# Optimization experiments

Measured on AMD Instinct MI355X. Metric: run time of the kernel, lower is better.

Reference implementation:

```python
import jax, jax.numpy as jnp
import numpy as np

EMB_DIM = 1024
SEQ = 2048
BATCH = 4


def setup_inputs() -> dict:
    key = jax.random.key(0)
    k1, k2, k3, k4, k5 = jax.random.split(key, 5)
    Q = jax.random.normal(k1, (SEQ, BATCH, EMB_DIM), dtype=jnp.float32)
    K = jax.random.normal(k2, (SEQ, BATCH, EMB_DIM), dtype=jnp.float32)
    V = jax.random.normal(k3, (SEQ, BATCH, EMB_DIM), dtype=jnp.float32)
    # nn.Linear default init scale ~ 1/sqrt(fan_in)
    W_in = jax.random.normal(k4, (3 * EMB_DIM, EMB_DIM), dtype=jnp.float32) / np.sqrt(EMB_DIM)
    W_out = jax.random.normal(k5, (EMB_DIM, EMB_DIM), dtype=jnp.float32) / np.sqrt(EMB_DIM)
    return {"Q": Q, "K": K, "V": V, "W_in": W_in, "W_out": W_out}


def reference(Q, K, V, W_in, W_out):
    # NOTE: original module ignores K and V args entirely (self-attention on Q).
    emb = Q.shape[-1]
    scale = 1.0 / np.sqrt(emb)
    qkv = jnp.einsum('sbe,fe->sbf', Q, W_in)        # [S, B, 3E]
    q, k, v = jnp.split(qkv, 3, axis=-1)            # each [S, B, E]
    q = jnp.transpose(q, (1, 0, 2)) * scale         # [B, S, E]
    k = jnp.transpose(k, (1, 0, 2))                 # [B, S, E]
    v = jnp.transpose(v, (1, 0, 2))                 # [B, S, E]
    scores = jnp.einsum('bte,bse->bts', q, k)       # [B, T, S]
    # per-target-row softmax over source dim == vectorized softmax on last axis
    weights = jax.nn.softmax(scores, axis=-1)       # [B, T, S]
    out = jnp.einsum('bts,bse->bte', weights, v)    # [B, T, E]
    out = jnp.transpose(out, (1, 0, 2))             # [T, B, E]
    out = jnp.einsum('tbe,fe->tbf', out, W_out)     # [T, B, E]
    return (out, weights)
```

## Files before the change

### kernel.cpp

```cpp
#include <hip/hip_runtime.h>
#include <stdint.h>

typedef unsigned short u16;
typedef __bf16 bf16_t;
typedef bf16_t bf16x8 __attribute__((ext_vector_type(8)));
typedef float f32x4 __attribute__((ext_vector_type(4)));
typedef u16 u16x4 __attribute__((ext_vector_type(4)));
typedef u16 u16x8 __attribute__((ext_vector_type(8)));

#define AS1 __attribute__((address_space(1)))
#define AS3 __attribute__((address_space(3)))

__device__ __forceinline__ u16 f2bf(float f) {
  union { float f; uint32_t u; } x; x.f = f;
  uint32_t u = x.u;
  return (u16)((u + 0x7fffu + ((u >> 16) & 1u)) >> 16);
}

__device__ __forceinline__ float bf2f(u16 b) {
  union { uint32_t u; float f; } x; x.u = ((uint32_t)b) << 16;
  return x.f;
}

__device__ __forceinline__ void gload_lds16(const void* g, void* lds) {
  __builtin_amdgcn_global_load_lds((const AS1 uint32_t*)g, (AS3 uint32_t*)lds, 16, 0, 0);
}

__device__ __forceinline__ void xcd_remap(int& bx, int& by, int& bz) {
  const int gx = gridDim.x, gy = gridDim.y;
  const int n = gx * gy * gridDim.z;
  const int lin = blockIdx.x + gx * (blockIdx.y + gy * blockIdx.z);
  const int q = n >> 3;
  const int work = (lin & 7) * q + (lin >> 3);
  bx = work % gx;
  const int t = work / gx;
  by = t % gy;
  bz = t / gy;
}

#define BARRIER() do { asm volatile("" ::: "memory"); \
                       __builtin_amdgcn_s_barrier();  \
                       asm volatile("" ::: "memory"); } while (0)

#define MQS(MQi, NQi, ASET, BSET)                                              \
  do {                                                                         \
    __builtin_amdgcn_s_setprio(1);                                             \
    _Pragma("unroll") for (int j_ = 0; j_ < 4; ++j_) {                         \
      _Pragma("unroll") for (int i_ = 0; i_ < 2; ++i_) {                       \
        acc[(MQi) * 4 + j_][(NQi) * 2 + i_] =                                  \
            __builtin_amdgcn_mfma_f32_16x16x32_bf16(                           \
                ASET[j_][0], BSET[i_][0],                                      \
                acc[(MQi) * 4 + j_][(NQi) * 2 + i_], 0, 0, 0);                 \
        acc[(MQi) * 4 + j_][(NQi) * 2 + i_] =                                  \
            __builtin_amdgcn_mfma_f32_16x16x32_bf16(                           \
                ASET[j_][1], BSET[i_][1],                                      \
                acc[(MQi) * 4 + j_][(NQi) * 2 + i_], 0, 0, 0);                 \
      }                                                                        \
    }                                                                          \
    __builtin_amdgcn_s_setprio(0);                                             \
  } while (0)

__global__ __launch_bounds__(256)
void cvt3(const float* __restrict__ Q, const float* __restrict__ Wi,
          const float* __restrict__ Wo, u16* __restrict__ Qb,
          u16* __restrict__ Wib, u16* __restrict__ Wob) {
  const int i = blockIdx.x * 256 + threadIdx.x;
  const float* src;
  u16* dst;
  int j;
  if (i < 2097152)            { src = Q;  dst = Qb;  j = i; }
  else if (i < 2883584)       { src = Wi; dst = Wib; j = i - 2097152; }
  else                        { src = Wo; dst = Wob; j = i - 2883584; }
  float4 v = ((const float4*)src)[j];
  u16x4 o = {f2bf(v.x), f2bf(v.y), f2bf(v.z), f2bf(v.w)};
  *(u16x4*)(dst + (size_t)j * 4) = o;
}

template <bool BF16OUT>
__global__ __launch_bounds__(512, 2)
void gemm256(const u16* __restrict__ A, const u16* __restrict__ B,
             void* __restrict__ Cv,
             int lda, int ldb, int ldc,
             long long sAz, long long sBz, long long sCz,
             int K, float alpha) {
  __shared__ u16 As[2][256 * 64];
  __shared__ u16 Bs[2][256 * 64];
  int bx, by, bz;
  xcd_remap(bx, by, bz);
  const int tid  = threadIdx.x;
  const int lane = tid & 63;
  const int wid  = tid >> 6;
  const int wr   = wid >> 2;
  const int wc   = wid & 3;
  const long long z = bz;
  const u16* Ab = A + z * sAz;
  const u16* Bb = B + z * sBz;
  const int rowBase = by * 256;
  const int colBase = bx * 256;
  const int nt = K >> 6;

  const int sRow   = tid >> 3;
  const int sChunk = (tid & 7) ^ (sRow & 7);
  const size_t ldaS = (size_t)lda, ldbS = (size_t)ldb;
  const u16* aS = Ab + (size_t)(rowBase + sRow) * ldaS + sChunk * 8;
  const u16* bS = Bb + (size_t)(colBase + sRow) * ldbS + sChunk * 8;

  const int fr = lane & 15;
  const int kx = lane >> 4;
  const int rx = lane & 7;

  f32x4 acc[8][4];
  const f32x4 zf = {0.f, 0.f, 0.f, 0.f};
#pragma unroll
  for (int m = 0; m < 8; ++m)
#pragma unroll
    for (int n = 0; n < 4; ++n) acc[m][n] = zf;

  bf16x8 Ara[4][2], Arb[4][2], Bra[2][2], Brb[2][2];

  auto stageA = [&](int buf, int h, int kt) {
    const u16* s = aS + (size_t)(h * 128) * ldaS + kt;
    char* d = ((char*)&As[buf][0]) + h * 16384 + tid * 16;
    gload_lds16(s, d);
    gload_lds16(s + 64 * ldaS, d + 8192);
  };
  auto stageB = [&](int buf, int h, int kt) {
    const u16* s = bS + (size_t)(h * 128) * ldbS + kt;
    char* d = ((char*)&Bs[buf][0]) + h * 16384 + tid * 16;
    gload_lds16(s, d);
    gload_lds16(s + 64 * ldbS, d + 8192);
  };
  auto ldsA = [&](int buf, int mq, bf16x8 (&dst)[4][2]) {
#pragma unroll
    for (int j = 0; j < 4; ++j) {
      const int row = mq * 128 + wr * 64 + j * 16 + fr;
#pragma unroll
      for (int k = 0; k < 2; ++k) {
        const int ch = ((k * 4 + kx) ^ rx) * 8;
        dst[j][k] = *(const bf16x8*)&As[buf][row * 64 + ch];
      }
    }
  };
  auto ldsB = [&](int buf, int nq, bf16x8 (&dst)[2][2]) {
#pragma unroll
    for (int i = 0; i < 2; ++i) {
      const int row = nq * 128 + i * 64 + wc * 16 + fr;
#pragma unroll
      for (int k = 0; k < 2; ++k) {
        const int ch = ((k * 4 + kx) ^ rx) * 8;
        dst[i][k] = *(const bf16x8*)&Bs[buf][row * 64 + ch];
      }
    }
  };

  stageA(0, 0, 0);
  stageA(0, 1, 0);
  stageB(0, 0, 0);
  stageB(0, 1, 0);
  asm volatile("s_waitcnt vmcnt(0)" ::: "memory");
  BARRIER();
  ldsA(0, 0, Ara);
  ldsB(0, 0, Bra);

  for (int t = 0; t < nt; ++t) {
    const int c = t & 1;
    const int kt1 = (t + 1) << 6;
    const bool s1 = (t + 1 < nt);
    ldsB(c, 1, Brb);
    ldsA(c, 1, Arb);
    if (s1) {
      stageA(1 - c, 0, kt1);
      stageA(1 - c, 1, kt1);
      stageB(1 - c, 0, kt1);
      stageB(1 - c, 1, kt1);
    }
    MQS(0, 0, Ara, Bra);
    MQS(0, 1, Ara, Brb);
    if (s1) {
      asm volatile("s_waitcnt lgkmcnt(0)" ::: "memory");
      asm volatile("s_waitcnt vmcnt(0)" ::: "memory");
      BARRIER();
      ldsA(1 - c, 0, Ara);
      __builtin_amdgcn_sched_barrier(0);
    }
    MQS(1, 0, Arb, Bra);
    if (s1) ldsB(1 - c, 0, Bra);
    MQS(1, 1, Arb, Brb);
  }

  const int r0 = (lane >> 4) * 4;
#pragma unroll
  for (int m = 0; m < 8; ++m) {
    const int grow = rowBase + (m >> 2) * 128 + wr * 64 + (m & 3) * 16 + r0;
#pragma unroll
    for (int jj = 0; jj < 4; ++jj) {
      const size_t rOff = (size_t)(grow + jj) * (size_t)ldc;
      if constexpr (BF16OUT) {
        u16* C = (u16*)Cv + z * sCz;
#pragma unroll
        for (int n = 0; n < 4; ++n) {
          const int gcol = colBase + (n >> 1) * 128 + (n & 1) * 64 + wc * 16 + fr;
          C[rOff + gcol] = f2bf(acc[m][n][jj] * alpha);
        }
      } else {
        float* C = (float*)Cv + z * sCz;
#pragma unroll
        for (int n = 0; n < 4; ++n) {
          const int gcol = colBase + (n >> 1) * 128 + (n & 1) * 64 + wc * 16 + fr;
          C[rOff + gcol] = acc[m][n][jj] * alpha;
        }
      }
    }
  }
}

template <bool BF16OUT>
__global__ __launch_bounds__(512, 2)
void gemm128(const u16* __restrict__ A, const u16* __restrict__ B,
             void* __restrict__ Cv,
             int lda, int ldb, int ldc,
             long long sAz, long long sBz, long long sCz,
             int K, float alpha) {
  __shared__ u16 As[2][128 * 64];
  __shared__ u16 Bs[2][256 * 64];
  int bx, by, bz;
  xcd_remap(bx, by, bz);
  const int tid  = threadIdx.x;
  const int lane = tid & 63;
  const int wid  = tid >> 6;
  const int wr   = wid >> 2;
  const int wc   = wid & 3;
  const long long z = bz;
  const u16* Ab = A + z * sAz;
  const u16* Bb = B + z * sBz;
  const int rowBase = by * 128;
  const int colBase = bx * 256;
  const int nt = K >> 6;

  const int sRow   = tid >> 3;
  const int sChunk = (tid & 7) ^ (sRow & 7);
  const size_t ldaS = (size_t)lda, ldbS = (size_t)ldb;
  const u16* aS = Ab + (size_t)(rowBase + sRow) * ldaS + sChunk * 8;
  const u16* bS = Bb + (size_t)(colBase + sRow) * ldbS + sChunk * 8;

  const int fr = lane & 15;
  const int kx = lane >> 4;
  const int rx = lane & 7;

  f32x4 acc[4][4];
  const f32x4 zf = {0.f, 0.f, 0.f, 0.f};
#pragma unroll
  for (int m = 0; m < 4; ++m)
#pragma unroll
    for (int n = 0; n < 4; ++n) acc[m][n] = zf;

  bf16x8 Ara[4][2], Arb[4][2], Bra[2][2], Brb[2][2];

  auto stageA = [&](int buf, int kt) {
    const u16* s = aS + kt;
    char* d = ((char*)&As[buf][0]) + tid * 16;
    gload_lds16(s, d);
    gload_lds16(s + 64 * ldaS, d + 8192);
  };
  auto stageB = [&](int buf, int h, int kt) {
    const u16* s = bS + (size_t)(h * 128) * ldbS + kt;
    char* d = ((char*)&Bs[buf][0]) + h * 16384 + tid * 16;
    gload_lds16(s, d);
    gload_lds16(s + 64 * ldbS, d + 8192);
  };
  auto ldsA = [&](int buf, bf16x8 (&dst)[4][2]) {
#pragma unroll
    for (int j = 0; j < 4; ++j) {
      const int row = wr * 64 + j * 16 + fr;
#pragma unroll
      for (int k = 0; k < 2; ++k) {
        const int ch = ((k * 4 + kx) ^ rx) * 8;
        dst[j][k] = *(const bf16x8*)&As[buf][row * 64 + ch];
      }
    }
  };
  auto ldsB = [&](int buf, int nq, bf16x8 (&dst)[2][2]) {
#pragma unroll
    for (int i = 0; i < 2; ++i) {
      const int row = nq * 128 + i * 64 + wc * 16 + fr;
#pragma unroll
      for (int k = 0; k < 2; ++k) {
        const int ch = ((k * 4 + kx) ^ rx) * 8;
        dst[i][k] = *(const bf16x8*)&Bs[buf][row * 64 + ch];
      }
    }
  };

  auto tile = [&](int t, int c, bf16x8 (&ACUR)[4][2], bf16x8 (&ANXT)[4][2]) {
    const int kt1 = (t + 1) << 6;
    const bool s1 = (t + 1 < nt);
    ldsB(c, 1, Brb);
    if (s1) {
      stageA(1 - c, kt1);
      stageB(1 - c, 0, kt1);
      stageB(1 - c, 1, kt1);
    }
    MQS(0, 0, ACUR, Bra);
    if (s1) {
      asm volatile("s_waitcnt lgkmcnt(0)" ::: "memory");
      asm volatile("s_waitcnt vmcnt(0)" ::: "memory");
      BARRIER();
      ldsA(1 - c, ANXT);
      ldsB(1 - c, 0, Bra);
      __builtin_amdgcn_sched_barrier(0);
    }
    MQS(0, 1, ACUR, Brb);
  };

  stageA(0, 0);
  stageB(0, 0, 0);
  stageB(0, 1, 0);
  asm volatile("s_waitcnt vmcnt(0)" ::: "memory");
  BARRIER();
  ldsA(0, Ara);
  ldsB(0, 0, Bra);

  for (int tt = 0; tt < nt; tt += 2) {
    tile(tt,     0, Ara, Arb);
    tile(tt + 1, 1, Arb, Ara);
  }

  const int r0 = (lane >> 4) * 4;
#pragma unroll
  for (int m = 0; m < 4; ++m) {
    const int grow = rowBase + wr * 64 + m * 16 + r0;
#pragma unroll
    for (int jj = 0; jj < 4; ++jj) {
      const size_t rOff = (size_t)(grow + jj) * (size_t)ldc;
      if constexpr (BF16OUT) {
        u16* C = (u16*)Cv + z * sCz;
#pragma unroll
        for (int n = 0; n < 4; ++n) {
          const int gcol = colBase + (n >> 1) * 128 + (n & 1) * 64 + wc * 16 + fr;
          C[rOff + gcol] = f2bf(acc[m][n][jj] * alpha);
        }
      } else {
        float* C = (float*)Cv + z * sCz;
#pragma unroll
        for (int n = 0; n < 4; ++n) {
          const int gcol = colBase + (n >> 1) * 128 + (n & 1) * 64 + wc * 16 + fr;
          C[rOff + gcol] = acc[m][n][jj] * alpha;
        }
      }
    }
  }
}

__global__ __launch_bounds__(256)
void softmax_rows(u16* __restrict__ sbf, float* __restrict__ wfp) {
  const size_t row = blockIdx.x;
  const int tid = threadIdx.x;
  u16* pb = sbf + row * 2048;
  u16x8 xb = *(const u16x8*)(pb + tid * 8);
  float x[8];
#pragma unroll
  for (int j = 0; j < 8; ++j) x[j] = bf2f(xb[j]);
  float m = x[0];
#pragma unroll
  for (int j = 1; j < 8; ++j) m = fmaxf(m, x[j]);
#pragma unroll
  for (int o = 32; o; o >>= 1) m = fmaxf(m, __shfl_xor(m, o, 64));
  __shared__ float red[8];
  if ((tid & 63) == 0) red[tid >> 6] = m;
  __syncthreads();
  m = fmaxf(fmaxf(red[0], red[1]), fmaxf(red[2], red[3]));
  float e[8];
  float s = 0.f;
#pragma unroll
  for (int j = 0; j < 8; ++j) { e[j] = expf(x[j] - m); s += e[j]; }
#pragma unroll
  for (int o = 32; o; o >>= 1) s += __shfl_xor(s, o, 64);
  if ((tid & 63) == 0) red[4 + (tid >> 6)] = s;
  __syncthreads();
  s = (red[4] + red[5]) + (red[6] + red[7]);
  const float inv = 1.0f / s;
  float w[8];
#pragma unroll
  for (int j = 0; j < 8; ++j) w[j] = e[j] * inv;
  float* pf = wfp + row * 2048;
  float4 o0 = {w[0], w[1], w[2], w[3]};
  float4 o1 = {w[4], w[5], w[6], w[7]};
  ((float4*)pf)[tid * 2] = o0;
  ((float4*)pf)[tid * 2 + 1] = o1;
  u16x8 ub;
#pragma unroll
  for (int j = 0; j < 8; ++j) ub[j] = f2bf(w[j]);
  *(u16x8*)(pb + tid * 8) = ub;
}

extern "C" void kernel_launch(void* const* d_in, const int* in_sizes, int n_in,
                              void* d_out, int out_size, void* d_ws, size_t ws_size,
                              hipStream_t stream) {
  const float* Q  = (const float*)d_in[0];
  const float* Wi = (const float*)d_in[3];
  const float* Wo = (const float*)d_in[4];
  float* out0    = (float*)d_out;
  float* weights = out0 + (size_t)2048 * 4 * 1024;

  char* ws = (char*)d_ws;
  u16* Qb   = (u16*)(ws);
  u16* Wib  = (u16*)(ws + ((size_t)16 << 20));
  u16* Wob  = (u16*)(ws + ((size_t)22 << 20));
  u16* qkvb = (u16*)(ws + ((size_t)24 << 20));
  u16* vwT  = (u16*)(ws + ((size_t)72 << 20));
  u16* wbf  = (u16*)(ws + ((size_t)88 << 20));

  cvt3<<<dim3(12288), dim3(256), 0, stream>>>(Q, Wi, Wo, Qb, Wib, Wob);

  gemm256<true><<<dim3(8, 32, 1), dim3(512), 0, stream>>>(
      Qb, Wib, (void*)qkvb, 1024, 1024, 3072, 0, 0, 0, 1024, 1.0f);

  gemm128<true><<<dim3(4, 64, 1), dim3(512), 0, stream>>>(
      Qb, Wib + (size_t)2048 * 1024, (void*)(qkvb + 2048),
      1024, 1024, 3072, 0, 0, 0, 1024, 1.0f);

  gemm256<true><<<dim3(8, 8, 4), dim3(512), 0, stream>>>(
      qkvb, qkvb + 1024, (void*)wbf, 12288, 12288, 2048,
      3072LL, 3072LL, 4194304LL, 1024, 0.03125f);

  gemm128<true><<<dim3(8, 8, 4), dim3(512), 0, stream>>>(
      Wob, qkvb + 2048, (void*)vwT, 1024, 12288, 2048,
      0LL, 3072LL, 2097152LL, 1024, 1.0f);

  softmax_rows<<<dim3(8192), dim3(256), 0, stream>>>(wbf, weights);

  gemm128<false><<<dim3(4, 16, 4), dim3(512), 0, stream>>>(
      wbf, vwT, (void*)out0, 2048, 2048, 4096,
      4194304LL, 2097152LL, 1024LL, 2048, 1.0f);
}
```

Before: 194.2 us.

## Fold V projection into output weights to skip V-projection GEMM

Precomputes a combined weight Wc = W_out · W_v (transposing W_v, running a split-K GEMM into fp32 partials, then reducing and converting to bf16). The per-batch vW^T GEMM then reads Q directly with Wc, so the separate V-projection GEMM over all tokens is dropped. It adds a small weight-only GEMM, a transpose and a reduce each call, and rounds the fused weight to bf16 once, which slightly changes numerics. Softmax is also moved earlier in the launch order.

```diff
diff --git a/kernel.cpp b/kernel.cpp
--- a/kernel.cpp
+++ b/kernel.cpp
@@ -74,6 +74,43 @@
   float4 v = ((const float4*)src)[j];
   u16x4 o = {f2bf(v.x), f2bf(v.y), f2bf(v.z), f2bf(v.w)};
   *(u16x4*)(dst + (size_t)j * 4) = o;
+}
+
+__global__ __launch_bounds__(256)
+void transpose_w(const u16* __restrict__ src, u16* __restrict__ dst) {
+  __shared__ u16 tile[64][72];
+  const int j0 = blockIdx.x * 64;
+  const int e0 = blockIdx.y * 64;
+  const int tid = threadIdx.x;
+  const int r  = tid >> 3;
+  const int c8 = (tid & 7) * 8;
+#pragma unroll
+  for (int p = 0; p < 2; ++p) {
+    const int j = j0 + p * 32 + r;
+    *(u16x8*)&tile[p * 32 + r][c8] =
+        *(const u16x8*)(src + (size_t)j * 1024 + e0 + c8);
+  }
+  __syncthreads();
+#pragma unroll
+  for (int p = 0; p < 2; ++p) {
+    const int e = p * 32 + r;
+    u16x8 v;
+#pragma unroll
+    for (int q = 0; q < 8; ++q) v[q] = tile[c8 + q][e];
+    *(u16x8*)(dst + (size_t)(e0 + e) * 1024 + j0 + c8) = v;
+  }
+}
+
+__global__ __launch_bounds__(256)
+void wc_reduce(const float* __restrict__ p, u16* __restrict__ wc) {
+  const int i = blockIdx.x * 256 + threadIdx.x;
+  float4 a = ((const float4*)p)[i];
+  float4 b = ((const float4*)p)[i + 262144];
+  float4 c = ((const float4*)p)[i + 524288];
+  float4 d = ((const float4*)p)[i + 786432];
+  u16x4 o = {f2bf(a.x + b.x + c.x + d.x), f2bf(a.y + b.y + c.y + d.y),
+             f2bf(a.z + b.z + c.z + d.z), f2bf(a.w + b.w + c.w + d.w)};
+  *(u16x4*)(wc + (size_t)i * 4) = o;
 }
 
 template <bool BF16OUT>
@@ -403,31 +440,39 @@
   float* weights = out0 + (size_t)2048 * 4 * 1024;
 
   char* ws = (char*)d_ws;
-  u16* Qb   = (u16*)(ws);
-  u16* Wib  = (u16*)(ws + ((size_t)16 << 20));
-  u16* Wob  = (u16*)(ws + ((size_t)22 << 20));
-  u16* qkvb = (u16*)(ws + ((size_t)24 << 20));
-  u16* vwT  = (u16*)(ws + ((size_t)72 << 20));
-  u16* wbf  = (u16*)(ws + ((size_t)88 << 20));
+  u16* Qb    = (u16*)(ws);
+  u16* Wib   = (u16*)(ws + ((size_t)16 << 20));
+  u16* Wob   = (u16*)(ws + ((size_t)22 << 20));
+  u16* Wc    = Wob;
+  u16* qkvb  = (u16*)(ws + ((size_t)24 << 20));
+  u16* WivT  = (u16*)(ws + ((size_t)72 << 20));
+  u16* vwT   = (u16*)(ws + ((size_t)72 << 20));
+  float* wcp = (float*)(ws + ((size_t)88 << 20));
+  u16* wbf   = (u16*)(ws + ((size_t)88 << 20));
 
   cvt3<<<dim3(12288), dim3(256), 0, stream>>>(Q, Wi, Wo, Qb, Wib, Wob);
+
+  transpose_w<<<dim3(16, 16), dim3(256), 0, stream>>>(
+      Wib + (size_t)2048 * 1024, WivT);
+
+  gemm128<false><<<dim3(4, 8, 4), dim3(512), 0, stream>>>(
+      Wob, WivT, (void*)wcp, 1024, 1024, 1024,
+      256LL, 256LL, 1048576LL, 256, 1.0f);
+
+  wc_reduce<<<dim3(1024), dim3(256), 0, stream>>>(wcp, Wc);
 
   gemm256<true><<<dim3(8, 32, 1), dim3(512), 0, stream>>>(
       Qb, Wib, (void*)qkvb, 1024, 1024, 3072, 0, 0, 0, 1024, 1.0f);
-
-  gemm128<true><<<dim3(4, 64, 1), dim3(512), 0, stream>>>(
-      Qb, Wib + (size_t)2048 * 1024, (void*)(qkvb + 2048),
-      1024, 1024, 3072, 0, 0, 0, 1024, 1.0f);
 
   gemm256<true><<<dim3(8, 8, 4), dim3(512), 0, stream>>>(
       qkvb, qkvb + 1024, (void*)wbf, 12288, 12288, 2048,
       3072LL, 3072LL, 4194304LL, 1024, 0.03125f);
 
+  softmax_rows<<<dim3(8192), dim3(256), 0, stream>>>(wbf, weights);
+
   gemm128<true><<<dim3(8, 8, 4), dim3(512), 0, stream>>>(
-      Wob, qkvb + 2048, (void*)vwT, 1024, 12288, 2048,
-      0LL, 3072LL, 2097152LL, 1024, 1.0f);
-
-  softmax_rows<<<dim3(8192), dim3(256), 0, stream>>>(wbf, weights);
+      Wc, Qb, (void*)vwT, 1024, 4096, 2048,
+      0LL, 1024LL, 2097152LL, 1024, 1.0f);
 
   gemm128<false><<<dim3(4, 16, 4), dim3(512), 0, stream>>>(
       wbf, vwT, (void*)out0, 2048, 2048, 4096,
```

After: 186.6 us. -3.9%, faster.
